# Optimization experiments

Hardware: AMD Instinct MI355X
Metric: run time of the kernel (lower is better)

## Reference

```python
import jax, jax.numpy as jnp
import numpy as np

N, M, K, D = 100000, 8, 256, 64  # batch, n_quantizer, n_codeword, len_subvec
LEN_VEC = M * D


def setup_inputs() -> dict:
    key = jax.random.key(0)
    k1, k2 = jax.random.split(key)
    x = jax.random.normal(k1, (N, LEN_VEC), dtype=jnp.float32)
    codebooks = jax.random.normal(k2, (M, K, D), dtype=jnp.float32)
    return {"x": x, "codebooks": codebooks, "soft_rate": -1}


def reference(x, codebooks, soft_rate):
    # x: [N, len_vec] -> [N, M, D] subvectors
    xs = x.reshape(x.shape[0], M, D)
    # squared L2 distances per (sample, quantizer, codeword): [N, M, K]
    x_sq = jnp.sum(xs * xs, axis=-1, keepdims=True)            # [N, M, 1]
    c_sq = jnp.sum(codebooks * codebooks, axis=-1)             # [M, K]
    cross = jnp.einsum('nmd,mkd->nmk', xs, codebooks)          # [N, M, K]
    dist = x_sq - 2.0 * cross + c_sq[None, :, :]               # [N, M, K]
    ids = jnp.argmin(dist, axis=-1)                            # [N, M]
    if soft_rate > 0:
        # soft assignment: convex combo of codewords weighted by softmax(-soft_rate * dist)
        w = jax.nn.softmax(-soft_rate * dist, axis=-1)         # [N, M, K]
        q = jnp.einsum('nmk,mkd->nmd', w, codebooks)           # [N, M, D]
    else:
        # hard assignment: gather nearest codeword per quantizer
        q = jnp.take_along_axis(codebooks[None], ids[:, :, None, None], axis=2)
        q = q[:, :, 0, :]                                      # [N, M, D]
    Q_x = q.reshape(-1, LEN_VEC)                               # [N, len_vec]
    id_x = ids.T.astype(jnp.int64)                             # [M, N], matches torch layout
    return Q_x, id_x
```

## Files before the change

### kernel.cpp

```cpp
#include <hip/hip_runtime.h>

#define NN 100000
#define MM 8
#define KK 256
#define DD 64
#define BROWS 128
#define NTILES ((NN + BROWS - 1) / BROWS)

typedef _Float16 half8 __attribute__((ext_vector_type(8)));
typedef float    f32x4 __attribute__((ext_vector_type(4)));


__global__ __launch_bounds__(256) void pq_prep_kernel(
    const float* __restrict__ cb, half8* __restrict__ whi,
    half8* __restrict__ wlo, float* __restrict__ csq)
{
    const int t = blockIdx.x * 256 + threadIdx.x;
    const int m = t >> 11, rest = t & 2047;
    const int c = rest >> 8, k = rest & 255;
    const float* src = cb + ((size_t)(m * KK + k)) * DD + c * 8;
    half8 h, l;
#pragma unroll
    for (int j = 0; j < 8; ++j) {
        float v = src[j];
        _Float16 hi = (_Float16)v;
        h[j] = hi;
        l[j] = (_Float16)((v - (float)hi) * 2048.0f);
    }
    whi[t] = h;
    wlo[t] = l;

    if (t < MM * KK) {
        const float* cr = cb + (size_t)t * DD;
        float s0 = 0.f, s1 = 0.f, s2 = 0.f, s3 = 0.f;
#pragma unroll
        for (int d = 0; d < DD; d += 4) {
            s0 = fmaf(cr[d + 0], cr[d + 0], s0);
            s1 = fmaf(cr[d + 1], cr[d + 1], s1);
            s2 = fmaf(cr[d + 2], cr[d + 2], s2);
            s3 = fmaf(cr[d + 3], cr[d + 3], s3);
        }
        csq[t] = (s0 + s1) + (s2 + s3);
    }
}

#define DELTA 4.0e-3f

__global__ __launch_bounds__(256, 4) void pq_main_kernel(
    const float* __restrict__ x, const half8* __restrict__ whi,
    const half8* __restrict__ wlo, const float* __restrict__ csqg,
    const float* __restrict__ cbf, float* __restrict__ qout,
    float* __restrict__ idout)
{
    __shared__ float csq_s[KK];
    __shared__ int   cand_k[BROWS];

    const int m   = blockIdx.y;
    const int n0  = blockIdx.x * BROWS;
    const int tid = threadIdx.x;
    const int w = tid >> 6, L = tid & 63;
    const int q = L >> 4, ci = L & 15;

    csq_s[tid] = csqg[m * KK + tid];

    half8 Ah[2][2], Al[2][2];
#pragma unroll
    for (int rb = 0; rb < 2; ++rb) {
        int n = n0 + w * 32 + rb * 16 + ci;
        if (n > NN - 1) n = NN - 1;
        const float4* xp = (const float4*)(x + (size_t)n * (MM * DD) + m * DD);
#pragma unroll
        for (int t = 0; t < 2; ++t) {
            float4 v0 = xp[t * 8 + q * 2 + 0];
            float4 v1 = xp[t * 8 + q * 2 + 1];
            float vs[8] = {v0.x, v0.y, v0.z, v0.w, v1.x, v1.y, v1.z, v1.w};
#pragma unroll
            for (int j = 0; j < 8; ++j) {
                _Float16 hi = (_Float16)vs[j];
                Ah[rb][t][j] = hi;
                Al[rb][t][j] = (_Float16)((vs[j] - (float)hi) * 2048.0f);
            }
        }
    }

    float d1v[2][4], d2v[2][4];
    int   k1v[2][4];
#pragma unroll
    for (int rb = 0; rb < 2; ++rb)
#pragma unroll
        for (int r = 0; r < 4; ++r) { d1v[rb][r] = 3.4e38f; d2v[rb][r] = 3.4e38f; k1v[rb][r] = 0; }

    const half8* bh0p = whi + m * 2048 + q * 256;
    const half8* bh1p = whi + m * 2048 + (4 + q) * 256;
    const half8* bl0p = wlo + m * 2048 + q * 256;
    const half8* bl1p = wlo + m * 2048 + (4 + q) * 256;

    __syncthreads();

    half8 bh0 = bh0p[ci], bh1 = bh1p[ci], bl0 = bl0p[ci], bl1 = bl1p[ci];

    for (int kt = 0; kt < 16; ++kt) {
        int kn = kt + 1; if (kn > 15) kn = 15;
        const int o = kn * 16 + ci;
        half8 nh0 = bh0p[o], nh1 = bh1p[o], nl0 = bl0p[o], nl1 = bl1p[o];

        f32x4 acc1[2], acc2[2];
        const f32x4 z = {0.f, 0.f, 0.f, 0.f};
        acc1[0] = z; acc1[1] = z; acc2[0] = z; acc2[1] = z;
#pragma unroll
        for (int rb = 0; rb < 2; ++rb) {
            acc1[rb] = __builtin_amdgcn_mfma_f32_16x16x32_f16(Ah[rb][0], bh0, acc1[rb], 0, 0, 0);
            acc1[rb] = __builtin_amdgcn_mfma_f32_16x16x32_f16(Ah[rb][1], bh1, acc1[rb], 0, 0, 0);
            acc2[rb] = __builtin_amdgcn_mfma_f32_16x16x32_f16(Ah[rb][0], bl0, acc2[rb], 0, 0, 0);
            acc2[rb] = __builtin_amdgcn_mfma_f32_16x16x32_f16(Ah[rb][1], bl1, acc2[rb], 0, 0, 0);
            acc2[rb] = __builtin_amdgcn_mfma_f32_16x16x32_f16(Al[rb][0], bh0, acc2[rb], 0, 0, 0);
            acc2[rb] = __builtin_amdgcn_mfma_f32_16x16x32_f16(Al[rb][1], bh1, acc2[rb], 0, 0, 0);
        }

        const int k = kt * 16 + ci;
        const float cq = csq_s[k];
#pragma unroll
        for (int rb = 0; rb < 2; ++rb)
#pragma unroll
            for (int r = 0; r < 4; ++r) {
                float cross = acc1[rb][r] + acc2[rb][r] * (1.0f / 2048.0f);
                float d = cq - 2.0f * cross;
                if (d < d1v[rb][r]) {
                    d2v[rb][r] = d1v[rb][r];
                    d1v[rb][r] = d; k1v[rb][r] = k;
                } else if (d < d2v[rb][r]) {
                    d2v[rb][r] = d;
                }
            }

        bh0 = nh0; bh1 = nh1; bl0 = nl0; bl1 = nl1;
    }

#pragma unroll
    for (int rb = 0; rb < 2; ++rb)
#pragma unroll
        for (int r = 0; r < 4; ++r) {
            float d = d1v[rb][r];
            int   k = k1v[rb][r];
            for (int mask = 1; mask < 16; mask <<= 1) {
                float ds = __shfl_xor(d, mask);
                int   ks = __shfl_xor(k, mask);
                if (ds < d || (ds == d && ks < k)) { d = ds; k = ks; }
            }
            const float thr = d + DELTA;
            int cnt = (d1v[rb][r] <= thr ? 1 : 0) + (d2v[rb][r] <= thr ? 1 : 0);
            for (int mask = 1; mask < 16; mask <<= 1) cnt += __shfl_xor(cnt, mask);

            const int n = n0 + w * 32 + rb * 16 + q * 4 + r;
            if (cnt > 1 && n < NN) {
                const float* xr = x + (size_t)n * (MM * DD) + m * DD;
                float s0 = 0.f, s1 = 0.f, s2 = 0.f, s3 = 0.f;
                for (int dd = 0; dd < DD; dd += 4) {
                    s0 = fmaf(xr[dd + 0], xr[dd + 0], s0);
                    s1 = fmaf(xr[dd + 1], xr[dd + 1], s1);
                    s2 = fmaf(xr[dd + 2], xr[dd + 2], s2);
                    s3 = fmaf(xr[dd + 3], xr[dd + 3], s3);
                }
                const float xsq = (s0 + s1) + (s2 + s3);
                float bd = 3.4e38f; int bk = 0;
                for (int j = 0; j < 16; ++j) {
                    const int kk = ci + 16 * j;
                    const float* c0 = cbf + ((size_t)(m * KK + kk)) * DD;
                    float a0 = 0.f, a1 = 0.f;
                    for (int dd = 0; dd < DD; dd += 2) {
                        a0 = fmaf(c0[dd + 0], xr[dd + 0], a0);
                        a1 = fmaf(c0[dd + 1], xr[dd + 1], a1);
                    }
                    const float dist = (xsq - 2.f * (a0 + a1)) + csq_s[kk];
                    if (dist < bd) { bd = dist; bk = kk; }
                }
                for (int mask = 1; mask < 16; mask <<= 1) {
                    float db = __shfl_xor(bd, mask);
                    int   kb = __shfl_xor(bk, mask);
                    if (db < bd || (db == bd && kb < bk)) { bd = db; bk = kb; }
                }
                k = bk;
            }
            if (ci == r) cand_k[w * 32 + rb * 16 + q * 4 + r] = k;
        }
    __syncthreads();

    if (tid < BROWS) {
        int n = n0 + tid;
        if (n < NN) idout[(size_t)m * NN + n] = (float)cand_k[tid];
    }
    for (int i = 0; i < 8; ++i) {
        int row = i * 16 + (tid >> 4);
        int n = n0 + row;
        if (n < NN) {
            int k = cand_k[row];
            int j = tid & 15;
            float4 v = ((const float4*)cbf)[(m * KK + k) * 16 + j];
            ((float4*)(qout + (size_t)n * (MM * DD) + m * DD))[j] = v;
        }
    }
}

extern "C" void kernel_launch(void* const* d_in, const int* in_sizes, int n_in,
                              void* d_out, int out_size, void* d_ws, size_t ws_size,
                              hipStream_t stream)
{
    const float* x  = (const float*)d_in[0];
    const float* cb = (const float*)d_in[1];

    float* qout  = (float*)d_out;
    float* idout = qout + (size_t)NN * (MM * DD);

    half8* whi = (half8*)d_ws;
    half8* wlo = (half8*)((char*)d_ws + 256 * 1024);
    float* csq = (float*)((char*)d_ws + 512 * 1024);

    pq_prep_kernel<<<dim3(64), dim3(256), 0, stream>>>(cb, whi, wlo, csq);

    pq_main_kernel<<<dim3(NTILES, MM), dim3(256), 0, stream>>>(
        x, whi, wlo, csq, cb, qout, idout);
}
```

Baseline: 424.3 us.

## Fully unroll codeword loop with triple-buffered prefetch and lower occupancy bound

Replaces the 16-iteration codebook tile loop with a fully unrolled sequence that prefetches codebook fragments two tiles ahead using three register buffers, and interleaves MFMAs across the two row blocks. This targets global-load latency stalls on the codebook fragments, which the single-stage prefetch only partly hid. The extra buffers raise register pressure, so launch bounds drop from 4 to 3 waves-per-SIMD minimum, which may lower occupancy.

```diff
diff --git a/kernel.cpp b/kernel.cpp
--- a/kernel.cpp
+++ b/kernel.cpp
@@ -46,7 +46,54 @@
 
 #define DELTA 4.0e-3f
 
-__global__ __launch_bounds__(256, 4) void pq_main_kernel(
+#define MFMA16(A, B, C) __builtin_amdgcn_mfma_f32_16x16x32_f16(A, B, C, 0, 0, 0)
+
+#define PF(P, KT)                                                          \
+    {                                                                      \
+        const int o_ = (KT) * 16 + ci;                                     \
+        P##h0 = bh0p[o_]; P##h1 = bh1p[o_];                                \
+        P##l0 = bl0p[o_]; P##l1 = bl1p[o_];                                \
+    }
+
+#define BODY(P, KT)                                                        \
+    {                                                                      \
+        f32x4 acc1_0 = z, acc1_1 = z, acc2_0 = z, acc2_1 = z;              \
+        acc1_0 = MFMA16(Ah[0][0], P##h0, acc1_0);                          \
+        acc1_0 = MFMA16(Ah[0][1], P##h1, acc1_0);                          \
+        acc2_0 = MFMA16(Ah[0][0], P##l0, acc2_0);                          \
+        acc2_0 = MFMA16(Ah[0][1], P##l1, acc2_0);                          \
+        acc2_0 = MFMA16(Al[0][0], P##h0, acc2_0);                          \
+        acc2_0 = MFMA16(Al[0][1], P##h1, acc2_0);                          \
+        acc1_1 = MFMA16(Ah[1][0], P##h0, acc1_1);                          \
+        acc1_1 = MFMA16(Ah[1][1], P##h1, acc1_1);                          \
+        acc2_1 = MFMA16(Ah[1][0], P##l0, acc2_1);                          \
+        acc2_1 = MFMA16(Ah[1][1], P##l1, acc2_1);                          \
+        acc2_1 = MFMA16(Al[1][0], P##h0, acc2_1);                          \
+        acc2_1 = MFMA16(Al[1][1], P##h1, acc2_1);                          \
+        const int k_ = (KT) * 16 + ci;                                     \
+        const float cq_ = csq_s[k_];                                       \
+        _Pragma("unroll")                                                  \
+        for (int r = 0; r < 4; ++r) {                                      \
+            float cross0 = acc1_0[r] + acc2_0[r] * (1.0f / 2048.0f);       \
+            float d0 = cq_ - 2.0f * cross0;                                \
+            if (d0 < d1v[0][r]) {                                          \
+                d2v[0][r] = d1v[0][r];                                     \
+                d1v[0][r] = d0; k1v[0][r] = k_;                            \
+            } else if (d0 < d2v[0][r]) {                                   \
+                d2v[0][r] = d0;                                            \
+            }                                                              \
+            float cross1 = acc1_1[r] + acc2_1[r] * (1.0f / 2048.0f);       \
+            float d1 = cq_ - 2.0f * cross1;                                \
+            if (d1 < d1v[1][r]) {                                          \
+                d2v[1][r] = d1v[1][r];                                     \
+                d1v[1][r] = d1; k1v[1][r] = k_;                            \
+            } else if (d1 < d2v[1][r]) {                                   \
+                d2v[1][r] = d1;                                            \
+            }                                                              \
+        }                                                                  \
+    }
+
+__global__ __launch_bounds__(256, 3) void pq_main_kernel(
     const float* __restrict__ x, const half8* __restrict__ whi,
     const half8* __restrict__ wlo, const float* __restrict__ csqg,
     const float* __restrict__ cbf, float* __restrict__ qout,
@@ -97,44 +144,31 @@
 
     __syncthreads();
 
-    half8 bh0 = bh0p[ci], bh1 = bh1p[ci], bl0 = bl0p[ci], bl1 = bl1p[ci];
-
-    for (int kt = 0; kt < 16; ++kt) {
-        int kn = kt + 1; if (kn > 15) kn = 15;
-        const int o = kn * 16 + ci;
-        half8 nh0 = bh0p[o], nh1 = bh1p[o], nl0 = bl0p[o], nl1 = bl1p[o];
-
-        f32x4 acc1[2], acc2[2];
-        const f32x4 z = {0.f, 0.f, 0.f, 0.f};
-        acc1[0] = z; acc1[1] = z; acc2[0] = z; acc2[1] = z;
-#pragma unroll
-        for (int rb = 0; rb < 2; ++rb) {
-            acc1[rb] = __builtin_amdgcn_mfma_f32_16x16x32_f16(Ah[rb][0], bh0, acc1[rb], 0, 0, 0);
-            acc1[rb] = __builtin_amdgcn_mfma_f32_16x16x32_f16(Ah[rb][1], bh1, acc1[rb], 0, 0, 0);
-            acc2[rb] = __builtin_amdgcn_mfma_f32_16x16x32_f16(Ah[rb][0], bl0, acc2[rb], 0, 0, 0);
-            acc2[rb] = __builtin_amdgcn_mfma_f32_16x16x32_f16(Ah[rb][1], bl1, acc2[rb], 0, 0, 0);
-            acc2[rb] = __builtin_amdgcn_mfma_f32_16x16x32_f16(Al[rb][0], bh0, acc2[rb], 0, 0, 0);
-            acc2[rb] = __builtin_amdgcn_mfma_f32_16x16x32_f16(Al[rb][1], bh1, acc2[rb], 0, 0, 0);
-        }
-
-        const int k = kt * 16 + ci;
-        const float cq = csq_s[k];
-#pragma unroll
-        for (int rb = 0; rb < 2; ++rb)
-#pragma unroll
-            for (int r = 0; r < 4; ++r) {
-                float cross = acc1[rb][r] + acc2[rb][r] * (1.0f / 2048.0f);
-                float d = cq - 2.0f * cross;
-                if (d < d1v[rb][r]) {
-                    d2v[rb][r] = d1v[rb][r];
-                    d1v[rb][r] = d; k1v[rb][r] = k;
-                } else if (d < d2v[rb][r]) {
-                    d2v[rb][r] = d;
-                }
-            }
-
-        bh0 = nh0; bh1 = nh1; bl0 = nl0; bl1 = nl1;
-    }
+    const f32x4 z = {0.f, 0.f, 0.f, 0.f};
+
+    half8 s0h0, s0h1, s0l0, s0l1;
+    half8 s1h0, s1h1, s1l0, s1l1;
+    half8 s2h0, s2h1, s2l0, s2l1;
+
+    PF(s0, 0)
+    PF(s1, 1)
+
+    PF(s2, 2)   BODY(s0, 0)
+    PF(s0, 3)   BODY(s1, 1)
+    PF(s1, 4)   BODY(s2, 2)
+    PF(s2, 5)   BODY(s0, 3)
+    PF(s0, 6)   BODY(s1, 4)
+    PF(s1, 7)   BODY(s2, 5)
+    PF(s2, 8)   BODY(s0, 6)
+    PF(s0, 9)   BODY(s1, 7)
+    PF(s1, 10)  BODY(s2, 8)
+    PF(s2, 11)  BODY(s0, 9)
+    PF(s0, 12)  BODY(s1, 10)
+    PF(s1, 13)  BODY(s2, 11)
+    PF(s2, 14)  BODY(s0, 12)
+    PF(s0, 15)  BODY(s1, 13)
+                BODY(s2, 14)
+                BODY(s0, 15)
 
 #pragma unroll
     for (int rb = 0; rb < 2; ++rb)
```

Measured after the change: 428.0 us. About the same (+0.9%).

## Halve rows per block, pack codeword index into distance bits for branchless top-2

Applied to the files above, without the earlier changes.

Cuts the rows per block from 128 to 64, so each wave handles one 16-row MFMA tile instead of two, and raises the launch-bounds occupancy hint from 4 to 6. The running top-2 search now stores the codeword tile index in the low 4 mantissa bits of the distance, which lets it use branchless fminf/fmaxf updates instead of compare-and-swap branches. The explicit next-tile prefetch of codebook fragments is dropped in favour of unroll-by-2. The aim is lower register pressure and higher occupancy with less divergent work in the inner loop. In exchange, codebook fragments are loaded twice as often per row, and the mantissa truncation perturbs distances slightly; the DELTA-based refine pass is there to absorb that.

```diff
diff --git a/kernel.cpp b/kernel.cpp
--- a/kernel.cpp
+++ b/kernel.cpp
@@ -4,7 +4,7 @@
 #define MM 8
 #define KK 256
 #define DD 64
-#define BROWS 128
+#define BROWS 64
 #define NTILES ((NN + BROWS - 1) / BROWS)
 
 typedef _Float16 half8 __attribute__((ext_vector_type(8)));
@@ -46,7 +46,9 @@
 
 #define DELTA 4.0e-3f
 
-__global__ __launch_bounds__(256, 4) void pq_main_kernel(
+#define MFMA16(A, B, C) __builtin_amdgcn_mfma_f32_16x16x32_f16(A, B, C, 0, 0, 0)
+
+__global__ __launch_bounds__(256, 6) void pq_main_kernel(
     const float* __restrict__ x, const half8* __restrict__ whi,
     const half8* __restrict__ wlo, const float* __restrict__ csqg,
     const float* __restrict__ cbf, float* __restrict__ qout,
@@ -63,10 +65,9 @@
 
     csq_s[tid] = csqg[m * KK + tid];
 
-    half8 Ah[2][2], Al[2][2];
-#pragma unroll
-    for (int rb = 0; rb < 2; ++rb) {
-        int n = n0 + w * 32 + rb * 16 + ci;
+    half8 Ah[2], Al[2];
+    {
+        int n = n0 + w * 16 + ci;
         if (n > NN - 1) n = NN - 1;
         const float4* xp = (const float4*)(x + (size_t)n * (MM * DD) + m * DD);
 #pragma unroll
@@ -77,18 +78,15 @@
 #pragma unroll
             for (int j = 0; j < 8; ++j) {
                 _Float16 hi = (_Float16)vs[j];
-                Ah[rb][t][j] = hi;
-                Al[rb][t][j] = (_Float16)((vs[j] - (float)hi) * 2048.0f);
-            }
-        }
-    }
-
-    float d1v[2][4], d2v[2][4];
-    int   k1v[2][4];
-#pragma unroll
-    for (int rb = 0; rb < 2; ++rb)
-#pragma unroll
-        for (int r = 0; r < 4; ++r) { d1v[rb][r] = 3.4e38f; d2v[rb][r] = 3.4e38f; k1v[rb][r] = 0; }
+                Ah[t][j] = hi;
+                Al[t][j] = (_Float16)((vs[j] - (float)hi) * 2048.0f);
+            }
+        }
+    }
+
+    float m1[4], m2[4];
+#pragma unroll
+    for (int r = 0; r < 4; ++r) { m1[r] = 3.4e38f; m2[r] = 3.4e38f; }
 
     const half8* bh0p = whi + m * 2048 + q * 256;
     const half8* bh1p = whi + m * 2048 + (4 + q) * 256;
@@ -97,99 +95,89 @@
 
     __syncthreads();
 
-    half8 bh0 = bh0p[ci], bh1 = bh1p[ci], bl0 = bl0p[ci], bl1 = bl1p[ci];
-
+    const f32x4 z = {0.f, 0.f, 0.f, 0.f};
+
+#pragma unroll 2
     for (int kt = 0; kt < 16; ++kt) {
-        int kn = kt + 1; if (kn > 15) kn = 15;
-        const int o = kn * 16 + ci;
-        half8 nh0 = bh0p[o], nh1 = bh1p[o], nl0 = bl0p[o], nl1 = bl1p[o];
-
-        f32x4 acc1[2], acc2[2];
-        const f32x4 z = {0.f, 0.f, 0.f, 0.f};
-        acc1[0] = z; acc1[1] = z; acc2[0] = z; acc2[1] = z;
-#pragma unroll
-        for (int rb = 0; rb < 2; ++rb) {
-            acc1[rb] = __builtin_amdgcn_mfma_f32_16x16x32_f16(Ah[rb][0], bh0, acc1[rb], 0, 0, 0);
-            acc1[rb] = __builtin_amdgcn_mfma_f32_16x16x32_f16(Ah[rb][1], bh1, acc1[rb], 0, 0, 0);
-            acc2[rb] = __builtin_amdgcn_mfma_f32_16x16x32_f16(Ah[rb][0], bl0, acc2[rb], 0, 0, 0);
-            acc2[rb] = __builtin_amdgcn_mfma_f32_16x16x32_f16(Ah[rb][1], bl1, acc2[rb], 0, 0, 0);
-            acc2[rb] = __builtin_amdgcn_mfma_f32_16x16x32_f16(Al[rb][0], bh0, acc2[rb], 0, 0, 0);
-            acc2[rb] = __builtin_amdgcn_mfma_f32_16x16x32_f16(Al[rb][1], bh1, acc2[rb], 0, 0, 0);
-        }
+        const int o = kt * 16 + ci;
+        half8 bh0 = bh0p[o], bh1 = bh1p[o], bl0 = bl0p[o], bl1 = bl1p[o];
+
+        f32x4 acc1 = z, acc2 = z;
+        acc1 = MFMA16(Ah[0], bh0, acc1);
+        acc1 = MFMA16(Ah[1], bh1, acc1);
+        acc2 = MFMA16(Ah[0], bl0, acc2);
+        acc2 = MFMA16(Ah[1], bl1, acc2);
+        acc2 = MFMA16(Al[0], bh0, acc2);
+        acc2 = MFMA16(Al[1], bh1, acc2);
 
         const int k = kt * 16 + ci;
         const float cq = csq_s[k];
 #pragma unroll
-        for (int rb = 0; rb < 2; ++rb)
-#pragma unroll
-            for (int r = 0; r < 4; ++r) {
-                float cross = acc1[rb][r] + acc2[rb][r] * (1.0f / 2048.0f);
-                float d = cq - 2.0f * cross;
-                if (d < d1v[rb][r]) {
-                    d2v[rb][r] = d1v[rb][r];
-                    d1v[rb][r] = d; k1v[rb][r] = k;
-                } else if (d < d2v[rb][r]) {
-                    d2v[rb][r] = d;
+        for (int r = 0; r < 4; ++r) {
+            float cross = acc1[r] + acc2[r] * (1.0f / 2048.0f);
+            float d = cq - 2.0f * cross;
+            unsigned du = __float_as_uint(d);
+            float key = __uint_as_float((du & 0xFFFFFFF0u) | (unsigned)kt);
+            float t2 = fmaxf(m1[r], key);
+            m2[r] = fminf(m2[r], t2);
+            m1[r] = fminf(m1[r], key);
+        }
+    }
+
+#pragma unroll
+    for (int r = 0; r < 4; ++r) {
+        float key = m1[r];
+        int   kk  = (int)(__float_as_uint(key) & 15u) * 16 + ci;
+        for (int mask = 1; mask < 16; mask <<= 1) {
+            float ks = __shfl_xor(key, mask);
+            int   kx = __shfl_xor(kk, mask);
+            if (ks < key || (ks == key && kx < kk)) { key = ks; kk = kx; }
+        }
+        const float thr = key + DELTA;
+        int cnt = (m1[r] <= thr ? 1 : 0) + (m2[r] <= thr ? 1 : 0);
+        for (int mask = 1; mask < 16; mask <<= 1) cnt += __shfl_xor(cnt, mask);
+
+        const int n = n0 + w * 16 + q * 4 + r;
+        int kfin = kk;
+        if (cnt > 1 && n < NN) {
+            const float* xr = x + (size_t)n * (MM * DD) + m * DD;
+            float s0 = 0.f, s1 = 0.f, s2 = 0.f, s3 = 0.f;
+            for (int dd = 0; dd < DD; dd += 4) {
+                s0 = fmaf(xr[dd + 0], xr[dd + 0], s0);
+                s1 = fmaf(xr[dd + 1], xr[dd + 1], s1);
+                s2 = fmaf(xr[dd + 2], xr[dd + 2], s2);
+                s3 = fmaf(xr[dd + 3], xr[dd + 3], s3);
+            }
+            const float xsq = (s0 + s1) + (s2 + s3);
+            float bd = 3.4e38f; int bk = 0;
+            for (int j = 0; j < 16; ++j) {
+                const int kc = ci + 16 * j;
+                const float* c0 = cbf + ((size_t)(m * KK + kc)) * DD;
+                float a0 = 0.f, a1 = 0.f;
+                for (int dd = 0; dd < DD; dd += 2) {
+                    a0 = fmaf(c0[dd + 0], xr[dd + 0], a0);
+                    a1 = fmaf(c0[dd + 1], xr[dd + 1], a1);
                 }
-            }
-
-        bh0 = nh0; bh1 = nh1; bl0 = nl0; bl1 = nl1;
-    }
-
-#pragma unroll
-    for (int rb = 0; rb < 2; ++rb)
-#pragma unroll
-        for (int r = 0; r < 4; ++r) {
-            float d = d1v[rb][r];
-            int   k = k1v[rb][r];
+                const float dist = (xsq - 2.f * (a0 + a1)) + csq_s[kc];
+                if (dist < bd) { bd = dist; bk = kc; }
+            }
             for (int mask = 1; mask < 16; mask <<= 1) {
-                float ds = __shfl_xor(d, mask);
-                int   ks = __shfl_xor(k, mask);
-                if (ds < d || (ds == d && ks < k)) { d = ds; k = ks; }
-            }
-            const float thr = d + DELTA;
-            int cnt = (d1v[rb][r] <= thr ? 1 : 0) + (d2v[rb][r] <= thr ? 1 : 0);
-            for (int mask = 1; mask < 16; mask <<= 1) cnt += __shfl_xor(cnt, mask);
-
-            const int n = n0 + w * 32 + rb * 16 + q * 4 + r;
-            if (cnt > 1 && n < NN) {
-                const float* xr = x + (size_t)n * (MM * DD) + m * DD;
-                float s0 = 0.f, s1 = 0.f, s2 = 0.f, s3 = 0.f;
-                for (int dd = 0; dd < DD; dd += 4) {
-                    s0 = fmaf(xr[dd + 0], xr[dd + 0], s0);
-                    s1 = fmaf(xr[dd + 1], xr[dd + 1], s1);
-                    s2 = fmaf(xr[dd + 2], xr[dd + 2], s2);
-                    s3 = fmaf(xr[dd + 3], xr[dd + 3], s3);
-                }
-                const float xsq = (s0 + s1) + (s2 + s3);
-                float bd = 3.4e38f; int bk = 0;
-                for (int j = 0; j < 16; ++j) {
-                    const int kk = ci + 16 * j;
-                    const float* c0 = cbf + ((size_t)(m * KK + kk)) * DD;
-                    float a0 = 0.f, a1 = 0.f;
-                    for (int dd = 0; dd < DD; dd += 2) {
-                        a0 = fmaf(c0[dd + 0], xr[dd + 0], a0);
-                        a1 = fmaf(c0[dd + 1], xr[dd + 1], a1);
-                    }
-                    const float dist = (xsq - 2.f * (a0 + a1)) + csq_s[kk];
-                    if (dist < bd) { bd = dist; bk = kk; }
-                }
-                for (int mask = 1; mask < 16; mask <<= 1) {
-                    float db = __shfl_xor(bd, mask);
-                    int   kb = __shfl_xor(bk, mask);
-                    if (db < bd || (db == bd && kb < bk)) { bd = db; bk = kb; }
-                }
-                k = bk;
-            }
-            if (ci == r) cand_k[w * 32 + rb * 16 + q * 4 + r] = k;
-        }
+                float db = __shfl_xor(bd, mask);
+                int   kb = __shfl_xor(bk, mask);
+                if (db < bd || (db == bd && kb < bk)) { bd = db; bk = kb; }
+            }
+            kfin = bk;
+        }
+        if (ci == r) cand_k[w * 16 + q * 4 + r] = kfin;
+    }
     __syncthreads();
 
     if (tid < BROWS) {
         int n = n0 + tid;
         if (n < NN) idout[(size_t)m * NN + n] = (float)cand_k[tid];
     }
-    for (int i = 0; i < 8; ++i) {
+#pragma unroll
+    for (int i = 0; i < 4; ++i) {
         int row = i * 16 + (tid >> 4);
         int n = n0 + row;
         if (n < NN) {
```

Result: slower. 499.2 us (+17.6%).
